# Kernel optimization log

Measured on AMD Instinct MI355X. Metric: run time of the kernel, lower is better.

## Reference

```python
import jax, jax.numpy as jnp
import numpy as np

B, T, D, E, P = 32, 8192, 256, 16, 64  # batch, tokens, dim, num_spectral_blocks, pixels_per_patch


def setup_inputs() -> dict:
    key = jax.random.key(0)
    k1, k2, k3, k4 = jax.random.split(key, 4)
    x = jax.random.normal(k1, (B, T, D), dtype=jnp.float32)
    block_indices = jax.random.randint(k2, (B, T), 0, E)
    # per-expert Linear(dim -> pixels_per_patch): weight [E, D, P], bias [E, P]
    W = jax.random.normal(k3, (E, D, P), dtype=jnp.float32) * 0.02
    b = jax.random.normal(k4, (E, P), dtype=jnp.float32) * 0.02
    return {"x": x, "W": W, "b": b, "block_indices": block_indices}


def reference(x, W, b, block_indices):
    # Each token [b, t] is routed to expert block_indices[b, t]; that expert's
    # Linear(dim -> pixels_per_patch) produces the output row. Loop is over the
    # small fixed expert count (16), fully vectorized over tokens.
    num_experts = W.shape[0]
    out = jnp.zeros(x.shape[:2] + (W.shape[2],), dtype=x.dtype)
    for e in range(num_experts):
        y = x @ W[e] + b[e]                       # [B, T, P]
        sel = (block_indices == e)[..., None]      # [B, T, 1]
        out = jnp.where(sel, y, out)
    return out
```

## Files before the change

### kernel.cpp

```cpp
#include <hip/hip_runtime.h>

#define NT (32 * 8192)
#define DIM 256
#define NE 16
#define NP 64
#define CAP 20480
#define NS 64

typedef short bf16x8 __attribute__((ext_vector_type(8)));
typedef float f32x4 __attribute__((ext_vector_type(4)));

__device__ __forceinline__ unsigned short f2bf(float f) {
  unsigned int u = __builtin_bit_cast(unsigned int, f);
  u += 0x7fffu + ((u >> 16) & 1u);
  return (unsigned short)(u >> 16);
}

__global__ void k_wconv(const float* __restrict__ W, unsigned short* __restrict__ Wt,
                        int* __restrict__ cnt) {
  if (blockIdx.x == 0 && threadIdx.x < NE) cnt[threadIdx.x] = 0;
  int gid = blockIdx.x * 256 + threadIdx.x;
  int e = gid >> 10;
  int n = (gid >> 4) & 63;
  int k0 = (gid & 15) << 4;
  const float* src = W + e * (DIM * NP) + n;
  unsigned short* dst = Wt + ((e * NP + n) * DIM + k0);
  #pragma unroll
  for (int j = 0; j < 16; ++j) dst[j] = f2bf(src[(k0 + j) * NP]);
}

__global__ void k_bucket(const int* __restrict__ idx, int* __restrict__ cnt,
                         int* __restrict__ bucket) {
  __shared__ int h[NE], base[NE], cur[NE];
  int t = threadIdx.x;
  if (t < NE) { h[t] = 0; cur[t] = 0; }
  __syncthreads();
  int b0 = blockIdx.x * 4096;
  int er[16];
  #pragma unroll
  for (int i = 0; i < 16; ++i) {
    er[i] = idx[b0 + i * 256 + t];
    atomicAdd(&h[er[i]], 1);
  }
  __syncthreads();
  if (t < NE) base[t] = atomicAdd(&cnt[t], h[t]);
  __syncthreads();
  #pragma unroll
  for (int i = 0; i < 16; ++i) {
    int e = er[i];
    int pos = atomicAdd(&cur[e], 1);
    int wpos = base[e] + pos;
    if (wpos < CAP) bucket[e * CAP + wpos] = b0 + i * 256 + t;
  }
}

__global__ __launch_bounds__(256, 2) void k_gemm(
    const float* __restrict__ x, const unsigned short* __restrict__ Wt,
    const float* __restrict__ bvec, const int* __restrict__ cnt,
    const int* __restrict__ bucket, float* __restrict__ out) {
  int e = blockIdx.x >> 6;
  int slice = blockIdx.x & 63;
  int w = threadIdx.x >> 6;
  int lane = threadIdx.x & 63;
  int cc = lane & 15, q = lane >> 4;

  int rows_e = cnt[e];
  int ntiles = (rows_e + 15) >> 4;
  int stream = slice * 4 + w;

  const unsigned short* wb = Wt + e * NP * DIM;
  bf16x8 bfr[4][8];
  #pragma unroll
  for (int nf = 0; nf < 4; ++nf) {
    int n = nf * 16 + cc;
    #pragma unroll
    for (int ks = 0; ks < 8; ++ks)
      bfr[nf][ks] = *(const bf16x8*)(wb + n * DIM + ks * 32 + q * 8);
  }
  float bias[4];
  #pragma unroll
  for (int nf = 0; nf < 4; ++nf) bias[nf] = bvec[e * NP + nf * 16 + cc];

  const int* bkt = bucket + e * CAP;

  for (int rt = stream; rt < ntiles; rt += 256) {
    int r0 = rt << 4;
    int rows = rows_e - r0;
    if (rows > 16) rows = 16;

    int myr = cc < rows ? cc : 0;
    int tok = bkt[r0 + myr];
    const float* xr = x + (long)tok * DIM + q * 8;

    f32x4 va[16];
    #pragma unroll
    for (int ks = 0; ks < 8; ++ks) {
      va[2 * ks]     = *(const f32x4*)(xr + ks * 32);
      va[2 * ks + 1] = *(const f32x4*)(xr + ks * 32 + 4);
    }

    f32x4 acc[4] = {{0.f,0.f,0.f,0.f},{0.f,0.f,0.f,0.f},
                    {0.f,0.f,0.f,0.f},{0.f,0.f,0.f,0.f}};
    #pragma unroll
    for (int ks = 0; ks < 8; ++ks) {
      bf16x8 a;
      #pragma unroll
      for (int j = 0; j < 4; ++j) {
        a[j]     = (short)f2bf(va[2 * ks][j]);
        a[4 + j] = (short)f2bf(va[2 * ks + 1][j]);
      }
      #pragma unroll
      for (int nf = 0; nf < 4; ++nf)
        acc[nf] = __builtin_amdgcn_mfma_f32_16x16x32_bf16(a, bfr[nf][ks], acc[nf], 0, 0, 0);
    }

    #pragma unroll
    for (int r = 0; r < 4; ++r) {
      int m = q * 4 + r;
      if (m < rows) {
        int tk = bkt[r0 + m];
        float* orow = out + (long)tk * NP + cc;
        #pragma unroll
        for (int nf = 0; nf < 4; ++nf) orow[nf * 16] = acc[nf][r] + bias[nf];
      }
    }
  }
}

extern "C" void kernel_launch(void* const* d_in, const int* in_sizes, int n_in,
                              void* d_out, int out_size, void* d_ws, size_t ws_size,
                              hipStream_t stream) {
  const float* x = (const float*)d_in[0];
  const float* W = (const float*)d_in[1];
  const float* b = (const float*)d_in[2];
  const int* idx = (const int*)d_in[3];
  float* out = (float*)d_out;

  int* ws = (int*)d_ws;
  int* cnt = ws;
  int* bucket = ws + 1024;
  unsigned short* Wt = (unsigned short*)(ws + 1024 + NE * CAP);

  k_wconv<<<64, 256, 0, stream>>>(W, Wt, cnt);
  k_bucket<<<64, 256, 0, stream>>>(idx, cnt, bucket);
  k_gemm<<<NE * NS, 256, 0, stream>>>(x, Wt, b, cnt, bucket, out);
}
```

Before: 422.1 us.

## Bucket tokens per expert and chunk, fusing weight conversion with bucketing

Weight conversion and token bucketing are merged into one prep kernel, so one launch goes away. Tokens are now bucketed per (expert, chunk) with local shared-memory counters, which drops the global atomic counter and the count zeroing. Each GEMM wave processes tiles only from its own chunk bucket. The fixed per-chunk capacity of 352 could silently drop tokens if a chunk exceeds it. Partial tiles also become more common, which wastes some MFMA work.

```diff
diff --git a/kernel.cpp b/kernel.cpp
--- a/kernel.cpp
+++ b/kernel.cpp
@@ -4,8 +4,8 @@
 #define DIM 256
 #define NE 16
 #define NP 64
-#define CAP 20480
-#define NS 64
+#define NCH 64
+#define CAPC 352
 
 typedef short bf16x8 __attribute__((ext_vector_type(8)));
 typedef float f32x4 __attribute__((ext_vector_type(4)));
@@ -16,47 +16,40 @@
   return (unsigned short)(u >> 16);
 }
 
-__global__ void k_wconv(const float* __restrict__ W, unsigned short* __restrict__ Wt,
-                        int* __restrict__ cnt) {
-  if (blockIdx.x == 0 && threadIdx.x < NE) cnt[threadIdx.x] = 0;
-  int gid = blockIdx.x * 256 + threadIdx.x;
-  int e = gid >> 10;
-  int n = (gid >> 4) & 63;
-  int k0 = (gid & 15) << 4;
-  const float* src = W + e * (DIM * NP) + n;
-  unsigned short* dst = Wt + ((e * NP + n) * DIM + k0);
-  #pragma unroll
-  for (int j = 0; j < 16; ++j) dst[j] = f2bf(src[(k0 + j) * NP]);
-}
-
-__global__ void k_bucket(const int* __restrict__ idx, int* __restrict__ cnt,
-                         int* __restrict__ bucket) {
-  __shared__ int h[NE], base[NE], cur[NE];
+__global__ void k_prep(const float* __restrict__ W, const int* __restrict__ idx,
+                       unsigned short* __restrict__ Wt, int* __restrict__ cnt_ec,
+                       int* __restrict__ bucket) {
   int t = threadIdx.x;
-  if (t < NE) { h[t] = 0; cur[t] = 0; }
+  if (blockIdx.x >= 64) {
+    int gid = (blockIdx.x - 64) * 256 + t;
+    int e = gid >> 10;
+    int n = (gid >> 4) & 63;
+    int k0 = (gid & 15) << 4;
+    const float* src = W + e * (DIM * NP) + n;
+    unsigned short* dst = Wt + ((e * NP + n) * DIM + k0);
+    #pragma unroll
+    for (int j = 0; j < 16; ++j) dst[j] = f2bf(src[(k0 + j) * NP]);
+    return;
+  }
+  __shared__ int cur[NE];
+  if (t < NE) cur[t] = 0;
   __syncthreads();
-  int b0 = blockIdx.x * 4096;
-  int er[16];
+  int c = blockIdx.x;
+  int b0 = c * 4096;
   #pragma unroll
   for (int i = 0; i < 16; ++i) {
-    er[i] = idx[b0 + i * 256 + t];
-    atomicAdd(&h[er[i]], 1);
+    int tok = b0 + i * 256 + t;
+    int e = idx[tok];
+    int pos = atomicAdd(&cur[e], 1);
+    if (pos < CAPC) bucket[(e * NCH + c) * CAPC + pos] = tok;
   }
   __syncthreads();
-  if (t < NE) base[t] = atomicAdd(&cnt[t], h[t]);
-  __syncthreads();
-  #pragma unroll
-  for (int i = 0; i < 16; ++i) {
-    int e = er[i];
-    int pos = atomicAdd(&cur[e], 1);
-    int wpos = base[e] + pos;
-    if (wpos < CAP) bucket[e * CAP + wpos] = b0 + i * 256 + t;
-  }
+  if (t < NE) cnt_ec[t * NCH + c] = cur[t] < CAPC ? cur[t] : CAPC;
 }
 
 __global__ __launch_bounds__(256, 2) void k_gemm(
     const float* __restrict__ x, const unsigned short* __restrict__ Wt,
-    const float* __restrict__ bvec, const int* __restrict__ cnt,
+    const float* __restrict__ bvec, const int* __restrict__ cnt_ec,
     const int* __restrict__ bucket, float* __restrict__ out) {
   int e = blockIdx.x >> 6;
   int slice = blockIdx.x & 63;
@@ -64,9 +57,13 @@
   int lane = threadIdx.x & 63;
   int cc = lane & 15, q = lane >> 4;
 
-  int rows_e = cnt[e];
-  int ntiles = (rows_e + 15) >> 4;
-  int stream = slice * 4 + w;
+  int s = slice * 4 + w;
+  int c = s >> 2;
+  int sub = s & 3;
+
+  int rows_ec = cnt_ec[e * NCH + c];
+  int ntiles = (rows_ec + 15) >> 4;
+  const int* bkt = bucket + (e * NCH + c) * CAPC;
 
   const unsigned short* wb = Wt + e * NP * DIM;
   bf16x8 bfr[4][8];
@@ -81,11 +78,9 @@
   #pragma unroll
   for (int nf = 0; nf < 4; ++nf) bias[nf] = bvec[e * NP + nf * 16 + cc];
 
-  const int* bkt = bucket + e * CAP;
-
-  for (int rt = stream; rt < ntiles; rt += 256) {
+  for (int rt = sub; rt < ntiles; rt += 4) {
     int r0 = rt << 4;
-    int rows = rows_e - r0;
+    int rows = rows_ec - r0;
     if (rows > 16) rows = 16;
 
     int myr = cc < rows ? cc : 0;
@@ -137,11 +132,10 @@
   float* out = (float*)d_out;
 
   int* ws = (int*)d_ws;
-  int* cnt = ws;
+  int* cnt_ec = ws;
   int* bucket = ws + 1024;
-  unsigned short* Wt = (unsigned short*)(ws + 1024 + NE * CAP);
+  unsigned short* Wt = (unsigned short*)(ws + 1024 + NE * NCH * CAPC);
 
-  k_wconv<<<64, 256, 0, stream>>>(W, Wt, cnt);
-  k_bucket<<<64, 256, 0, stream>>>(idx, cnt, bucket);
-  k_gemm<<<NE * NS, 256, 0, stream>>>(x, Wt, b, cnt, bucket, out);
+  k_prep<<<128, 256, 0, stream>>>(W, idx, Wt, cnt_ec, bucket);
+  k_gemm<<<NE * 64, 256, 0, stream>>>(x, Wt, b, cnt_ec, bucket, out);
 }
```

Result: no change. 420.8 us (-0.3%).
